# Performance work log

Hardware: AMD Instinct MI355X
Metric: run time of the kernel (lower is better)

## Reference

```python
import jax, jax.numpy as jnp
import numpy as np

K = 16            # neighbors
RATIO = 0.25      # sampling ratio -> M = N*RATIO
EPS = 1e-5        # BatchNorm eps


def _fps(pts, m):
    # Farthest point sampling for one cloud. pts: (N,3) -> (m,) int32 indices.
    n = pts.shape[0]

    def body(carry, _):
        dist, last = carry                      # dist: (N,) min sq-dist to selected set
        d = jnp.sum((pts - pts[last]) ** 2, axis=-1)
        dist = jnp.minimum(dist, d)
        nxt = jnp.argmax(dist).astype(jnp.int32)
        return (dist, nxt), nxt

    init = (jnp.full((n,), jnp.inf, pts.dtype), jnp.int32(0))
    _, rest = jax.lax.scan(body, init, None, length=m - 1)
    return jnp.concatenate([jnp.zeros((1,), jnp.int32), rest])


def setup_inputs() -> dict:
    key = jax.random.key(0)
    ks = jax.random.split(key, 3)
    B, N, C_IN, C_OUT = 8, 8192, 64, 128
    x = jax.random.normal(ks[0], (B, N, C_IN), jnp.float32)
    p = jax.random.normal(ks[1], (B, N, 3), jnp.float32)
    W = jax.random.normal(ks[2], (C_OUT, C_IN), jnp.float32) * 0.05
    gamma = jnp.ones((C_OUT,), jnp.float32)
    beta = jnp.zeros((C_OUT,), jnp.float32)
    run_mean = jnp.zeros((C_OUT,), jnp.float32)
    run_var = jnp.ones((C_OUT,), jnp.float32)
    return {"x": x, "p": p, "W": W, "gamma": gamma, "beta": beta,
            "run_mean": run_mean, "run_var": run_var}


def reference(x, p, W, gamma, beta, run_mean, run_var):
    B, N, _ = x.shape
    M = int(N * RATIO)

    # 1) FPS sample M points per cloud
    idx_fps = jax.vmap(lambda q: _fps(q, M))(p)                   # (B, M)
    p_out = jnp.take_along_axis(p, idx_fps[..., None], axis=1)    # (B, M, 3)

    # 2) KNN: squared distances (B, M, N), sorted K nearest via top_k on -dist
    d2 = (jnp.sum(p_out ** 2, -1)[..., None]
          + jnp.sum(p ** 2, -1)[:, None, :]
          - 2.0 * jnp.einsum('bmd,bnd->bmn', p_out, p))
    _, nbr = jax.lax.top_k(-d2, K)                                # (B, M, K) ascending dist

    # 3) Pointwise MLP: Conv1d(k=1, no bias) == matmul, then BN (eval) + ReLU
    h = jnp.einsum('bnc,oc->bno', x, W)                           # (B, N, C_OUT)
    h = (h - run_mean) * jax.lax.rsqrt(run_var + EPS) * gamma + beta
    h = jax.nn.relu(h)

    # 4) Gather neighbor features and max-pool over K
    flat = nbr.reshape(B, M * K)
    feats = jnp.take_along_axis(h, flat[..., None], axis=1).reshape(B, M, K, -1)
    y = jnp.max(feats, axis=2)                                    # (B, M, C_OUT)
    return y, p_out
```

## Files before the change

### kernel.cpp

```cpp
#include <hip/hip_runtime.h>

#define B_   8
#define N_   8192
#define CIN  64
#define COUT 128
#define M_   2048
#define K_   16

typedef float v2f __attribute__((ext_vector_type(2)));

template <int CTRL>
__device__ __forceinline__ unsigned long long dpp64(unsigned long long x) {
  int lo = (int)(unsigned)(x & 0xFFFFFFFFull);
  int hi = (int)(unsigned)(x >> 32);
  int dlo = __builtin_amdgcn_update_dpp(lo, lo, CTRL, 0xF, 0xF, false);
  int dhi = __builtin_amdgcn_update_dpp(hi, hi, CTRL, 0xF, 0xF, false);
  return ((unsigned long long)(unsigned)dhi << 32) | (unsigned)dlo;
}

__device__ __forceinline__ unsigned long long readlane_u64(unsigned long long k, int l) {
  unsigned lo = (unsigned)__builtin_amdgcn_readlane((int)(unsigned)(k & 0xFFFFFFFFull), l);
  unsigned hi = (unsigned)__builtin_amdgcn_readlane((int)(unsigned)(k >> 32), l);
  return ((unsigned long long)hi << 32) | lo;
}

__device__ __forceinline__ unsigned long long wave_min_u64(unsigned long long k) {
  unsigned long long t;
  t = dpp64<0x111>(k); k = t < k ? t : k;
  t = dpp64<0x112>(k); k = t < k ? t : k;
  t = dpp64<0x114>(k); k = t < k ? t : k;
  t = dpp64<0x118>(k); k = t < k ? t : k;
  t = dpp64<0x142>(k); k = t < k ? t : k;
  t = dpp64<0x143>(k); k = t < k ? t : k;
  return readlane_u64(k, 63);
}

#define FTH 512
#define FPT 16
#define MROWS2 32

__global__ __launch_bounds__(512) void fps_mlp_kernel(
    const float* __restrict__ p, float* __restrict__ p_out,
    const float* __restrict__ x, const float* __restrict__ W,
    const float* __restrict__ gamma, const float* __restrict__ beta,
    const float* __restrict__ rmean, const float* __restrict__ rvar,
    float* __restrict__ h) {
#pragma clang fp contract(off)
  __shared__ __align__(16) unsigned char smem[139776];

  const int tid = threadIdx.x;

  if (blockIdx.x >= 8) {
    float* wt = (float*)smem;
    float* xs = (float*)(smem + 33792);

    const int o  = tid & 127;
    const int rg = tid >> 7;
    const int rowBase = (blockIdx.x - 8) * MROWS2;

    for (int idx = tid; idx < COUT * CIN; idx += 512) {
      const int oo = idx >> 6, cc = idx & 63;
      wt[cc * 132 + oo] = W[idx];
    }
    ((float4*)xs)[tid] = ((const float4*)(x + (size_t)rowBase * CIN))[tid];
    __syncthreads();

    float acc[8] = {0.f, 0.f, 0.f, 0.f, 0.f, 0.f, 0.f, 0.f};
#pragma unroll
    for (int c4 = 0; c4 < CIN / 4; c4++) {
      const float w0 = wt[(4 * c4 + 0) * 132 + o];
      const float w1 = wt[(4 * c4 + 1) * 132 + o];
      const float w2 = wt[(4 * c4 + 2) * 132 + o];
      const float w3 = wt[(4 * c4 + 3) * 132 + o];
#pragma unroll
      for (int i = 0; i < 8; i++) {
        const float4 xv = *(const float4*)&xs[(rg * 8 + i) * CIN + c4 * 4];
        acc[i] += xv.x * w0 + xv.y * w1 + xv.z * w2 + xv.w * w3;
      }
    }
    const float mu = rmean[o];
    const float sc = rsqrtf(rvar[o] + 1e-5f) * gamma[o];
    const float bt = beta[o];
#pragma unroll
    for (int i = 0; i < 8; i++) {
      const float v = (acc[i] - mu) * sc + bt;
      h[(size_t)(rowBase + rg * 8 + i) * COUT + o] = fmaxf(v, 0.f);
    }
    return;
  }

  float4* pc4 = (float4*)smem;
  unsigned long long (*wred)[8] =
      (unsigned long long (*)[8])(smem + 131072);
  int* idxHist = (int*)(smem + 131072 + 128);

  const int b  = blockIdx.x;
  const int wv = tid >> 6;
  const int ln = tid & 63;

  const float* pb = p + (size_t)b * N_ * 3;
  for (int n = tid; n < N_; n += FTH)
    pc4[n] = make_float4(pb[3 * n + 0], pb[3 * n + 1], pb[3 * n + 2], 0.f);
  if (tid == 0) idxHist[0] = 0;
  __syncthreads();

  float4 c0 = pc4[0];
  float cx = c0.x, cy = c0.y, cz = c0.z;

  v2f X2[8], Y2[8], Z2[8], D2[8];
#pragma unroll
  for (int j = 0; j < 8; j++) {
    float4 a = pc4[tid + (2 * j) * FTH];
    float4 c = pc4[tid + (2 * j + 1) * FTH];
    X2[j] = (v2f){a.x, c.x};
    Y2[j] = (v2f){a.y, c.y};
    Z2[j] = (v2f){a.z, c.z};
    D2[j] = (v2f){__builtin_inff(), __builtin_inff()};
  }

  unsigned lo32[16];
#pragma unroll
  for (int e = 0; e < 16; e++) lo32[e] = (unsigned)(N_ - 1 - tid - (e << 9));

  int buf = 0;
  for (int it = 1; it < M_; ++it) {
    const v2f cxv = {cx, cx}, cyv = {cy, cy}, czv = {cz, cz};
    unsigned long long kp[8];
#pragma unroll
    for (int j = 0; j < 8; j++) {
      v2f dx = X2[j] - cxv;
      v2f dy = Y2[j] - cyv;
      v2f dz = Z2[j] - czv;
      v2f m1 = dx * dx;
      v2f m2 = dy * dy;
      v2f s  = m1 + m2;
      v2f m3 = dz * dz;
      v2f d  = s + m3;
      v2f dm = __builtin_elementwise_min(D2[j], d);
      D2[j] = dm;
      const unsigned long long ka =
          ((unsigned long long)__float_as_uint(dm.x) << 32) | (unsigned long long)lo32[2 * j];
      const unsigned long long kb =
          ((unsigned long long)__float_as_uint(dm.y) << 32) | (unsigned long long)lo32[2 * j + 1];
      kp[j] = ka > kb ? ka : kb;
    }
    const unsigned long long q0 = kp[0] > kp[1] ? kp[0] : kp[1];
    const unsigned long long q1 = kp[2] > kp[3] ? kp[2] : kp[3];
    const unsigned long long q2 = kp[4] > kp[5] ? kp[4] : kp[5];
    const unsigned long long q3 = kp[6] > kp[7] ? kp[6] : kp[7];
    const unsigned long long h0 = q0 > q1 ? q0 : q1;
    const unsigned long long h1 = q2 > q3 ? q2 : q3;
    unsigned long long key = h0 > h1 ? h0 : h1;

    {
      unsigned long long t;
      t = dpp64<0x111>(key); key = t > key ? t : key;
      t = dpp64<0x112>(key); key = t > key ? t : key;
      t = dpp64<0x114>(key); key = t > key ? t : key;
      t = dpp64<0x118>(key); key = t > key ? t : key;
      t = dpp64<0x142>(key); key = t > key ? t : key;
      t = dpp64<0x143>(key); key = t > key ? t : key;
    }
    if (ln == 63) wred[buf][wv] = key;
    __syncthreads();
    unsigned long long kk = wred[buf][ln & 7];
    unsigned long long t;
    t = dpp64<0x111>(kk); kk = t > kk ? t : kk;
    t = dpp64<0x112>(kk); kk = t > kk ? t : kk;
    t = dpp64<0x114>(kk); kk = t > kk ? t : kk;
    const int nw = N_ - 1 -
        (int)(unsigned)__builtin_amdgcn_readlane((int)(unsigned)(kk & 0xFFFFFFFFull), 7);
    float4 cc = pc4[nw];
    cx = cc.x; cy = cc.y; cz = cc.z;
    if (tid == 0) idxHist[it] = nw;
    buf ^= 1;
  }
  __syncthreads();

  float* po = p_out + (size_t)b * M_ * 3;
  for (int mi = tid; mi < M_; mi += FTH) {
    float4 v = pc4[idxHist[mi]];
    po[mi * 3 + 0] = v.x;
    po[mi * 3 + 1] = v.y;
    po[mi * 3 + 2] = v.z;
  }
}

#define UMAXK 0xFFFFFFFFFFFFFFFFull
#define QPB  16

__global__ __launch_bounds__(1024) void knn_kernel(
    const float* __restrict__ p, const float* __restrict__ p_out,
    const float* __restrict__ h, float* __restrict__ y) {
#pragma clang fp contract(off)
  __shared__ float4 pc4[N_];
  __shared__ int winLds[QPB][K_];

  const int t    = threadIdx.x;
  const int wv   = t >> 6;
  const int lane = t & 63;
  const int b    = blockIdx.x & 7;
  const int grp  = blockIdx.x >> 3;
  const int q    = b * M_ + grp * QPB + wv;

  const float* pb = p + (size_t)b * N_ * 3;
  for (int n = t; n < N_; n += 1024) {
    float xx = pb[3 * n + 0], yy = pb[3 * n + 1], zz = pb[3 * n + 2];
    float sn = (xx * xx + yy * yy) + zz * zz;
    pc4[n] = make_float4(xx, yy, zz, sn);
  }
  __syncthreads();

  const float qx = p_out[q * 3 + 0];
  const float qy = p_out[q * 3 + 1];
  const float qz = p_out[q * 3 + 2];
  const float sq = (qx * qx + qy * qy) + qz * qz;

  unsigned long long c0 = UMAXK, c1 = UMAXK, c2 = UMAXK, c3 = UMAXK;
#pragma unroll 4
  for (int j = 0; j < 128; j++) {
    const int n = lane + (j << 6);
    float4 v = pc4[n];
    float dot = __builtin_fmaf(qz, v.z,
                __builtin_fmaf(qy, v.y, qx * v.x));
    float d2 = (sq + v.w) - 2.0f * dot;
    unsigned u = __float_as_uint(d2);
    u ^= (unsigned)((int)u >> 31) | 0x80000000u;
    unsigned long long key = ((unsigned long long)u << 32) | (unsigned)n;
    if (key < c3) {
      unsigned long long x2 = key, mn;
      mn = x2 < c0 ? x2 : c0; x2 = x2 < c0 ? c0 : x2; c0 = mn;
      mn = x2 < c1 ? x2 : c1; x2 = x2 < c1 ? c1 : x2; c1 = mn;
      mn = x2 < c2 ? x2 : c2; x2 = x2 < c2 ? c2 : x2; c2 = mn;
      c3 = x2 < c3 ? x2 : c3;
    }
  }

  int count = 4;
  unsigned long long em0 = 0ull, em1 = 0ull;
  unsigned long long mykey = UMAXK;

  for (int k = 0; k < K_; k++) {
    unsigned long long cnd = (count > 0) ? c0 : UMAXK;
    unsigned long long win = wave_min_u64(cnd);
    if (lane == k) mykey = win;
    const int nstar = (int)(unsigned)(win & 0xFFFFFFFFu);
    if ((nstar & 63) == lane) {
      const int j = nstar >> 6;
      if (j < 64) em0 |= 1ull << j; else em1 |= 1ull << (j - 64);
      c0 = c1; c1 = c2; c2 = c3; c3 = UMAXK; count--;
      if (count == 0 && k < K_ - 1) {
        c0 = c1 = c2 = c3 = UMAXK;
        for (int j2 = 0; j2 < 128; j2++) {
          bool ex = (j2 < 64) ? ((em0 >> j2) & 1ull) : ((em1 >> (j2 - 64)) & 1ull);
          if (!ex) {
            const int n2 = lane + (j2 << 6);
            float4 v = pc4[n2];
            float dot = __builtin_fmaf(qz, v.z,
                        __builtin_fmaf(qy, v.y, qx * v.x));
            float d2 = (sq + v.w) - 2.0f * dot;
            unsigned u = __float_as_uint(d2);
            u ^= (unsigned)((int)u >> 31) | 0x80000000u;
            unsigned long long kk2 = ((unsigned long long)u << 32) | (unsigned)n2;
            if (kk2 < c3) {
              unsigned long long x2 = kk2, mn;
              mn = x2 < c0 ? x2 : c0; x2 = x2 < c0 ? c0 : x2; c0 = mn;
              mn = x2 < c1 ? x2 : c1; x2 = x2 < c1 ? c1 : x2; c1 = mn;
              mn = x2 < c2 ? x2 : c2; x2 = x2 < c2 ? c2 : x2; c2 = mn;
              c3 = x2 < c3 ? x2 : c3;
            }
          }
        }
        count = 4;
      }
    }
  }

  if (lane < K_) winLds[wv][lane] = (int)(unsigned)(mykey & 0xFFFFFFFFu);
  __syncthreads();

  const float* hb = h + (size_t)b * N_ * COUT;
  float2 acc = make_float2(-__builtin_inff(), -__builtin_inff());
#pragma unroll
  for (int i = 0; i < K_; i++) {
    const int n = winLds[wv][i];
    float2 v = *(const float2*)(hb + (size_t)n * COUT + lane * 2);
    acc.x = fmaxf(acc.x, v.x);
    acc.y = fmaxf(acc.y, v.y);
  }
  *(float2*)(y + (size_t)q * COUT + lane * 2) = acc;
}

extern "C" void kernel_launch(void* const* d_in, const int* in_sizes, int n_in,
                              void* d_out, int out_size, void* d_ws, size_t ws_size,
                              hipStream_t stream) {
  const float* x     = (const float*)d_in[0];
  const float* p     = (const float*)d_in[1];
  const float* W     = (const float*)d_in[2];
  const float* gamma = (const float*)d_in[3];
  const float* beta  = (const float*)d_in[4];
  const float* rmean = (const float*)d_in[5];
  const float* rvar  = (const float*)d_in[6];

  float* y     = (float*)d_out;
  float* p_out = y + (size_t)B_ * M_ * COUT;
  float* h     = (float*)d_ws;

  fps_mlp_kernel<<<8 + (B_ * N_) / MROWS2, 512, 0, stream>>>(
      p, p_out, x, W, gamma, beta, rmean, rvar, h);
  knn_kernel<<<B_ * (M_ / QPB), 1024, 0, stream>>>(p, p_out, h, y);
}
```

Baseline: 2.170 ms.

## Halve FPS block to 256 threads and track argmax with float compare

FPS blocks shrink from 512 to 256 threads, so each thread holds 32 points and the cross-wave reduction covers 4 waves instead of 8, which shortens the per-iteration barrier and reduction chain. The per-point 64-bit key max is replaced by a float compare that tracks the best slot index, building a single 64-bit key only once per thread. The MLP blocks drop to 16 rows each, doubling their block count. This adds register pressure and serial work per thread in the FPS loop, and the MLP path's row-group indexing (tid>>7) may no longer match the smaller row count per block.

```diff
diff --git a/kernel.cpp b/kernel.cpp
--- a/kernel.cpp
+++ b/kernel.cpp
@@ -35,11 +35,11 @@
   return readlane_u64(k, 63);
 }
 
-#define FTH 512
-#define FPT 16
-#define MROWS2 32
-
-__global__ __launch_bounds__(512) void fps_mlp_kernel(
+#define FTH 256
+#define FPT 32
+#define MROWS2 16
+
+__global__ __launch_bounds__(256) void fps_mlp_kernel(
     const float* __restrict__ p, float* __restrict__ p_out,
     const float* __restrict__ x, const float* __restrict__ W,
     const float* __restrict__ gamma, const float* __restrict__ beta,
@@ -58,7 +58,7 @@
     const int rg = tid >> 7;
     const int rowBase = (blockIdx.x - 8) * MROWS2;
 
-    for (int idx = tid; idx < COUT * CIN; idx += 512) {
+    for (int idx = tid; idx < COUT * CIN; idx += 256) {
       const int oo = idx >> 6, cc = idx & 63;
       wt[cc * 132 + oo] = W[idx];
     }
@@ -107,9 +107,9 @@
   float4 c0 = pc4[0];
   float cx = c0.x, cy = c0.y, cz = c0.z;
 
-  v2f X2[8], Y2[8], Z2[8], D2[8];
-#pragma unroll
-  for (int j = 0; j < 8; j++) {
+  v2f X2[16], Y2[16], Z2[16], D2[16];
+#pragma unroll
+  for (int j = 0; j < 16; j++) {
     float4 a = pc4[tid + (2 * j) * FTH];
     float4 c = pc4[tid + (2 * j + 1) * FTH];
     X2[j] = (v2f){a.x, c.x};
@@ -118,16 +118,13 @@
     D2[j] = (v2f){__builtin_inff(), __builtin_inff()};
   }
 
-  unsigned lo32[16];
-#pragma unroll
-  for (int e = 0; e < 16; e++) lo32[e] = (unsigned)(N_ - 1 - tid - (e << 9));
-
   int buf = 0;
   for (int it = 1; it < M_; ++it) {
     const v2f cxv = {cx, cx}, cyv = {cy, cy}, czv = {cz, cz};
-    unsigned long long kp[8];
-#pragma unroll
-    for (int j = 0; j < 8; j++) {
+    v2f vbd = (v2f){-1.0f, -1.0f};
+    int sx = 0, sy = 1;
+#pragma unroll
+    for (int j = 0; j < 16; j++) {
       v2f dx = X2[j] - cxv;
       v2f dy = Y2[j] - cyv;
       v2f dz = Z2[j] - czv;
@@ -138,19 +135,19 @@
       v2f d  = s + m3;
       v2f dm = __builtin_elementwise_min(D2[j], d);
       D2[j] = dm;
-      const unsigned long long ka =
-          ((unsigned long long)__float_as_uint(dm.x) << 32) | (unsigned long long)lo32[2 * j];
-      const unsigned long long kb =
-          ((unsigned long long)__float_as_uint(dm.y) << 32) | (unsigned long long)lo32[2 * j + 1];
-      kp[j] = ka > kb ? ka : kb;
-    }
-    const unsigned long long q0 = kp[0] > kp[1] ? kp[0] : kp[1];
-    const unsigned long long q1 = kp[2] > kp[3] ? kp[2] : kp[3];
-    const unsigned long long q2 = kp[4] > kp[5] ? kp[4] : kp[5];
-    const unsigned long long q3 = kp[6] > kp[7] ? kp[6] : kp[7];
-    const unsigned long long h0 = q0 > q1 ? q0 : q1;
-    const unsigned long long h1 = q2 > q3 ? q2 : q3;
-    unsigned long long key = h0 > h1 ? h0 : h1;
+      const bool gx = dm.x > vbd.x;
+      const bool gy = dm.y > vbd.y;
+      sx = gx ? (2 * j) : sx;
+      sy = gy ? (2 * j + 1) : sy;
+      vbd = __builtin_elementwise_max(vbd, dm);
+    }
+    float bd; int bk;
+    if (vbd.y > vbd.x || (vbd.y == vbd.x && sy < sx)) { bd = vbd.y; bk = sy; }
+    else                                               { bd = vbd.x; bk = sx; }
+    const int n = tid + (bk << 8);
+    unsigned long long key =
+        ((unsigned long long)__float_as_uint(bd) << 32) |
+        (unsigned)(N_ - 1 - n);
 
     {
       unsigned long long t;
@@ -163,13 +160,12 @@
     }
     if (ln == 63) wred[buf][wv] = key;
     __syncthreads();
-    unsigned long long kk = wred[buf][ln & 7];
+    unsigned long long kk = wred[buf][ln & 3];
     unsigned long long t;
     t = dpp64<0x111>(kk); kk = t > kk ? t : kk;
     t = dpp64<0x112>(kk); kk = t > kk ? t : kk;
-    t = dpp64<0x114>(kk); kk = t > kk ? t : kk;
     const int nw = N_ - 1 -
-        (int)(unsigned)__builtin_amdgcn_readlane((int)(unsigned)(kk & 0xFFFFFFFFull), 7);
+        (int)(unsigned)__builtin_amdgcn_readlane((int)(unsigned)(kk & 0xFFFFFFFFull), 3);
     float4 cc = pc4[nw];
     cx = cc.x; cy = cc.y; cz = cc.z;
     if (tid == 0) idxHist[it] = nw;
@@ -306,7 +302,7 @@
   float* p_out = y + (size_t)B_ * M_ * COUT;
   float* h     = (float*)d_ws;
 
-  fps_mlp_kernel<<<8 + (B_ * N_) / MROWS2, 512, 0, stream>>>(
+  fps_mlp_kernel<<<8 + (B_ * N_) / MROWS2, 256, 0, stream>>>(
       p, p_out, x, W, gamma, beta, rmean, rvar, h);
   knn_kernel<<<B_ * (M_ / QPB), 1024, 0, stream>>>(p, p_out, h, y);
 }
```

Result: faster. 1.988 ms (-8.4%).
